# Kernel tuning notes

Measured on AMD Instinct MI355X. Metric: run time of the kernel, lower is better.

## Reference

```python
import jax, jax.numpy as jnp
import numpy as np

NEG_INF = -1e6  # d2l masked_softmax fill value


def setup_inputs() -> dict:
    key = jax.random.key(0)
    ks = jax.random.split(key, 7)
    B, Q, K, D, H = 16, 64, 512, 256, 256
    querys = jax.random.normal(ks[0], (B, Q, D), dtype=jnp.float32)
    keys = jax.random.normal(ks[1], (B, K, D), dtype=jnp.float32)
    values = jax.random.normal(ks[2], (B, K, D), dtype=jnp.float32)
    valid_lens = jax.random.randint(ks[3], (B,), 1, K + 1)
    # learned parameters (Linear weights stored as (in, out) for x @ W)
    Wq = jax.random.normal(ks[4], (D, H), dtype=jnp.float32) / np.sqrt(D)
    Wk = jax.random.normal(ks[5], (D, H), dtype=jnp.float32) / np.sqrt(D)
    w_v = jax.random.normal(ks[6], (H,), dtype=jnp.float32) / np.sqrt(H)
    return {"querys": querys, "keys": keys, "values": values,
            "valid_lens": valid_lens, "Wq": Wq, "Wk": Wk, "w_v": w_v}


def reference(querys, keys, values, valid_lens, Wq, Wk, w_v):
    B, Q, _ = querys.shape
    K = keys.shape[1]
    q = querys @ Wq                      # (B, Q, H)
    k = keys @ Wk                        # (B, K, H)
    features = jnp.tanh(q[:, :, None, :] + k[:, None, :, :])   # (B, Q, K, H)
    scores = jnp.einsum('bqkh,h->bqk', features, w_v)           # (B, Q, K)
    # masked softmax over key axis: positions >= valid_len get -1e6
    mask = jnp.arange(K)[None, None, :] < valid_lens[:, None, None]  # (B,1,K)
    scores = jnp.where(mask, scores, NEG_INF)
    attn = jax.nn.softmax(scores, axis=-1)                       # (B, Q, K)
    return jnp.einsum('bqk,bkd->bqd', attn, values)              # (B, Q, D)
```

## Files before the change

kernel.cpp:

```cpp
#include <hip/hip_runtime.h>

#define BB 16
#define QQ 64
#define KK 512
#define DD 256
#define HH 256
#define KTILE 128
#define NZ 4
#define PERSIST 2048
#define LDST 56

#define LOG2E2 2.88539008177792681f

typedef unsigned int uint;
typedef unsigned short ushort;
typedef __attribute__((ext_vector_type(8))) short bf16x8;
typedef __attribute__((ext_vector_type(8))) unsigned short ushort8;
typedef __attribute__((ext_vector_type(4))) float f32x4;

__device__ __forceinline__ float fast_exp2(float x) {
#if __has_builtin(__builtin_amdgcn_exp2f)
    return __builtin_amdgcn_exp2f(x);
#else
    return exp2f(x);
#endif
}

__device__ __forceinline__ ushort f32_to_bf16_rtne(float x) {
    uint u = __float_as_uint(x);
    u = (u + 0x7FFFu + ((u >> 16) & 1u)) >> 16;
    return (ushort)u;
}

__device__ __forceinline__ void cvt8(uint4 u, float4& a, float4& b) {
    a.x = __uint_as_float(u.x << 16); a.y = __uint_as_float(u.x & 0xFFFF0000u);
    a.z = __uint_as_float(u.y << 16); a.w = __uint_as_float(u.y & 0xFFFF0000u);
    b.x = __uint_as_float(u.z << 16); b.y = __uint_as_float(u.z & 0xFFFF0000u);
    b.z = __uint_as_float(u.w << 16); b.w = __uint_as_float(u.w & 0xFFFF0000u);
}

__global__ __launch_bounds__(256) void proj_both(
        const float* __restrict__ Xq, const float* __restrict__ Wq, float* __restrict__ Yq,
        const float* __restrict__ Xk, const float* __restrict__ Wk, ushort* __restrict__ Yk16,
        const int* __restrict__ valid_lens) {
    __shared__ ushort As[64 * LDST];
    __shared__ ushort Bt[64 * LDST];
    const int rt = blockIdx.x;
    const bool is_q = (rt < 16);
    const float* X; const float* W; int row0;
    if (is_q) { X = Xq; W = Wq; row0 = rt * 64; }
    else {
        X = Xk; W = Wk; row0 = (rt - 16) * 64;
        const int bb    = row0 >> 9;
        const int local = row0 & 511;
        if (local >= valid_lens[bb]) return;
    }
    const int col0 = blockIdx.y * 64;
    const int tid  = threadIdx.x;
    const int lane = tid & 63;
    const int w    = tid >> 6;

    f32x4 acc[4] = {{0.f,0.f,0.f,0.f}, {0.f,0.f,0.f,0.f},
                    {0.f,0.f,0.f,0.f}, {0.f,0.f,0.f,0.f}};

    const int ar = tid >> 2;
    const int ak = (tid & 3) * 8;
    const int bc = tid & 15;
    const int bk = tid >> 4;

    for (int k0 = 0; k0 < HH; k0 += 32) {
        {
            const float* xp = X + (size_t)(row0 + ar) * HH + k0 + ak;
            float4 x0 = *(const float4*)(xp);
            float4 x1 = *(const float4*)(xp + 4);
            ushort8 o;
            o[0] = f32_to_bf16_rtne(x0.x); o[1] = f32_to_bf16_rtne(x0.y);
            o[2] = f32_to_bf16_rtne(x0.z); o[3] = f32_to_bf16_rtne(x0.w);
            o[4] = f32_to_bf16_rtne(x1.x); o[5] = f32_to_bf16_rtne(x1.y);
            o[6] = f32_to_bf16_rtne(x1.z); o[7] = f32_to_bf16_rtne(x1.w);
            *(ushort8*)(&As[ar * LDST + ak]) = o;
        }
        {
            #pragma unroll
            for (int s = 0; s < 2; ++s) {
                float4 wv = *(const float4*)(W + (size_t)(k0 + bk + 16*s) * HH + col0 + bc*4);
                Bt[(bc*4 + 0) * LDST + bk + 16*s] = f32_to_bf16_rtne(wv.x);
                Bt[(bc*4 + 1) * LDST + bk + 16*s] = f32_to_bf16_rtne(wv.y);
                Bt[(bc*4 + 2) * LDST + bk + 16*s] = f32_to_bf16_rtne(wv.z);
                Bt[(bc*4 + 3) * LDST + bk + 16*s] = f32_to_bf16_rtne(wv.w);
            }
        }
        __syncthreads();

        const bf16x8 af = *(const bf16x8*)(&As[(w*16 + (lane & 15)) * LDST + (lane >> 4) * 8]);
        #pragma unroll
        for (int ct = 0; ct < 4; ++ct) {
            const bf16x8 bf = *(const bf16x8*)(&Bt[(ct*16 + (lane & 15)) * LDST + (lane >> 4) * 8]);
            acc[ct] = __builtin_amdgcn_mfma_f32_16x16x32_bf16(af, bf, acc[ct], 0, 0, 0);
        }
        __syncthreads();
    }

    const int orow = row0 + w*16 + (lane >> 4) * 4;
    const int ocol = col0 + (lane & 15);
    if (is_q) {
        #pragma unroll
        for (int ct = 0; ct < 4; ++ct)
            #pragma unroll
            for (int j = 0; j < 4; ++j)
                Yq[(size_t)(orow + j) * HH + ocol + ct*16] = acc[ct][j] * LOG2E2;
    } else {
        #pragma unroll
        for (int ct = 0; ct < 4; ++ct)
            #pragma unroll
            for (int j = 0; j < 4; ++j)
                Yk16[(size_t)(orow + j) * HH + ocol + ct*16] =
                    f32_to_bf16_rtne(acc[ct][j] * LOG2E2);
    }
}

__global__ __launch_bounds__(256) void fused_flash(
        const float* __restrict__ qf, const ushort* __restrict__ kf16,
        const float* __restrict__ w_v, const int* __restrict__ valid_lens,
        const float* __restrict__ values,
        float* __restrict__ pm, float* __restrict__ pl, float* __restrict__ po) {
    __shared__ float sc[2][KTILE];
    __shared__ float pp[2][KTILE];
    __shared__ float red[4][2][DD];

    const int tid  = threadIdx.x;
    const int lane = tid & 63;
    const int w    = tid >> 6;
    const int hg   = lane & 15;
    const int ksub = lane >> 4;
    const int h0   = hg * 16;

    float4 nw[4];
    float wvsum = 0.f;
    #pragma unroll
    for (int i = 0; i < 4; ++i) {
        float4 wv4 = *(const float4*)(w_v + h0 + i*4);
        wvsum += ((wv4.x + wv4.y) + (wv4.z + wv4.w));
        nw[i] = make_float4(-2.f*wv4.x, -2.f*wv4.y, -2.f*wv4.z, -2.f*wv4.w);
    }

    int TT = 0;
    #pragma unroll
    for (int i = 0; i < BB; ++i)
        TT += (valid_lens[i] + KTILE - 1) >> 7;
    const int items = TT * 32;
    const int qch   = items >> 11;
    const int rch   = items & 2047;
    const int bid   = blockIdx.x;
    const int lo_it = bid * qch + ((bid < rch) ? bid : rch);
    const int n_it  = qch + ((bid < rch) ? 1 : 0);

    for (int t = lo_it; t < lo_it + n_it; ++t) {
        const int tile_idx = t >> 5;
        const int q0       = (t & 31) * 2;

        int bb = 0, zz = 0, vlb = 1, acc = 0;
        #pragma unroll
        for (int i = 0; i < BB; ++i) {
            const int v   = valid_lens[i];
            const int nzi = (v + KTILE - 1) >> 7;
            const bool hit = (tile_idx >= acc) && (tile_idx < acc + nzi);
            if (hit) { bb = i; zz = tile_idx - acc; vlb = v; }
            acc += nzi;
        }

        const int tile_lo = zz * KTILE;
        const int tile_hi = (tile_lo + KTILE < vlb) ? (tile_lo + KTILE) : vlb;

        sc[tid >> 7][tid & 127] = -1e6f;

        float4 qA[4], qB[4];
        {
            const float* qrA = qf + (size_t)(bb*QQ + q0) * HH + h0;
            const float* qrB = qrA + HH;
            #pragma unroll
            for (int i = 0; i < 4; ++i) {
                qA[i] = *(const float4*)(qrA + i*4);
                qB[i] = *(const float4*)(qrB + i*4);
            }
        }

        const int lo  = tile_lo + w * 32;
        int hi = lo + 32; hi = (hi > tile_hi) ? tile_hi : hi;
        const int cnt = hi - lo;
        const int ng  = (cnt <= 0) ? 0 : ((cnt + 3) >> 2);

        __syncthreads();

        {
            const size_t brows = (size_t)bb * KK;
            uint4 c0, c1;
            if (ng > 0) {
                int row = lo + ksub;
                row = (row < tile_hi) ? row : (tile_hi - 1);
                const ushort* p = kf16 + (brows + row) * HH + h0;
                c0 = *(const uint4*)(p);
                c1 = *(const uint4*)(p + 8);
            }
            for (int g = 0; g < ng; ++g) {
                uint4 n0, n1;
                const bool more = (g + 1 < ng);
                if (more) {
                    int row = lo + (g+1)*4 + ksub;
                    row = (row < tile_hi) ? row : (tile_hi - 1);
                    const ushort* p = kf16 + (brows + row) * HH + h0;
                    n0 = *(const uint4*)(p);
                    n1 = *(const uint4*)(p + 8);
                }
                float4 kv[4];
                cvt8(c0, kv[0], kv[1]);
                cvt8(c1, kv[2], kv[3]);

                float a0 = wvsum, a1 = 0.f, a2 = 0.f, a3 = 0.f;
                float b0 = wvsum, b1 = 0.f, b2 = 0.f, b3 = 0.f;
                #pragma unroll
                for (int i = 0; i < 4; ++i) {
                    float eA0 = fast_exp2(qA[i].x + kv[i].x);
                    float eA1 = fast_exp2(qA[i].y + kv[i].y);
                    float eA2 = fast_exp2(qA[i].z + kv[i].z);
                    float eA3 = fast_exp2(qA[i].w + kv[i].w);
                    a0 = fmaf(nw[i].x, __builtin_amdgcn_rcpf(eA0 + 1.f), a0);
                    a1 = fmaf(nw[i].y, __builtin_amdgcn_rcpf(eA1 + 1.f), a1);
                    a2 = fmaf(nw[i].z, __builtin_amdgcn_rcpf(eA2 + 1.f), a2);
                    a3 = fmaf(nw[i].w, __builtin_amdgcn_rcpf(eA3 + 1.f), a3);
                    float eB0 = fast_exp2(qB[i].x + kv[i].x);
                    float eB1 = fast_exp2(qB[i].y + kv[i].y);
                    float eB2 = fast_exp2(qB[i].z + kv[i].z);
                    float eB3 = fast_exp2(qB[i].w + kv[i].w);
                    b0 = fmaf(nw[i].x, __builtin_amdgcn_rcpf(eB0 + 1.f), b0);
                    b1 = fmaf(nw[i].y, __builtin_amdgcn_rcpf(eB1 + 1.f), b1);
                    b2 = fmaf(nw[i].z, __builtin_amdgcn_rcpf(eB2 + 1.f), b2);
                    b3 = fmaf(nw[i].w, __builtin_amdgcn_rcpf(eB3 + 1.f), b3);
                }
                float sA = (a0 + a1) + (a2 + a3);
                float sB = (b0 + b1) + (b2 + b3);
                #pragma unroll
                for (int off = 8; off; off >>= 1) {
                    sA += __shfl_xor(sA, off);
                    sB += __shfl_xor(sB, off);
                }
                const int k = lo + g*4 + ksub;
                if (hg == 0 && k < hi) {
                    sc[0][k - tile_lo] = sA;
                    sc[1][k - tile_lo] = sB;
                }
                if (more) { c0 = n0; c1 = n1; }
            }
        }
        __syncthreads();

        if (w < 2) {
            float s0 = sc[w][lane*2], s1 = sc[w][lane*2 + 1];
            float m = fmaxf(s0, s1);
            #pragma unroll
            for (int off = 32; off; off >>= 1) m = fmaxf(m, __shfl_xor(m, off));
            float p0 = __expf(s0 - m), p1 = __expf(s1 - m);
            float l = p0 + p1;
            #pragma unroll
            for (int off = 32; off; off >>= 1) l += __shfl_xor(l, off);
            pp[w][lane*2]     = p0;
            pp[w][lane*2 + 1] = p1;
            if (lane == 0) {
                const int id = ((bb*QQ + q0 + w) << 2) + zz;
                pm[id] = m; pl[id] = l;
            }
        }
        __syncthreads();

        {
            const float* V = values + (size_t)bb * KK * DD + lane*4;
            float4 aA = make_float4(0.f,0.f,0.f,0.f);
            float4 aB = aA;
            #pragma unroll 4
            for (int k = lo; k < hi; ++k) {
                const float pA = pp[0][k - tile_lo];
                const float pB = pp[1][k - tile_lo];
                float4 v4 = *(const float4*)(V + (size_t)k * DD);
                aA.x = fmaf(pA, v4.x, aA.x); aA.y = fmaf(pA, v4.y, aA.y);
                aA.z = fmaf(pA, v4.z, aA.z); aA.w = fmaf(pA, v4.w, aA.w);
                aB.x = fmaf(pB, v4.x, aB.x); aB.y = fmaf(pB, v4.y, aB.y);
                aB.z = fmaf(pB, v4.z, aB.z); aB.w = fmaf(pB, v4.w, aB.w);
            }
            *(float4*)(&red[w][0][lane*4]) = aA;
            *(float4*)(&red[w][1][lane*4]) = aB;
        }
        __syncthreads();

        #pragma unroll
        for (int i = 0; i < 2; ++i) {
            const int idx = tid + i*256;
            const int qq = idx >> 8, d = idx & 255;
            const float o = (red[0][qq][d] + red[1][qq][d])
                          + (red[2][qq][d] + red[3][qq][d]);
            po[(size_t)(((bb*QQ + q0 + qq) << 2) + zz) * DD + d] = o;
        }
        __syncthreads();
    }
}

__global__ __launch_bounds__(256) void combine_kernel(
        const float* __restrict__ pm, const float* __restrict__ pl,
        const float* __restrict__ po, const int* __restrict__ valid_lens,
        float* __restrict__ out) {
    const int b   = blockIdx.x;
    const int q   = blockIdx.y;
    const int tid = threadIdx.x;
    const int vl  = valid_lens[b];
    const int nz  = (vl + KTILE - 1) >> 7;
    const int idx4 = (b*QQ + q) << 2;

    float mz[NZ], wz[NZ];
    float M = -3.0e38f;
    #pragma unroll
    for (int z = 0; z < NZ; ++z) {
        mz[z] = (z < nz) ? pm[idx4 + z] : -3.0e38f;
        M = fmaxf(M, mz[z]);
    }
    float L = 0.f;
    #pragma unroll
    for (int z = 0; z < NZ; ++z) {
        wz[z] = (z < nz) ? __expf(mz[z] - M) : 0.f;
        L = fmaf(wz[z], (z < nz) ? pl[idx4 + z] : 0.f, L);
    }
    const float inv = 1.f / L;

    float o = 0.f;
    #pragma unroll
    for (int z = 0; z < NZ; ++z) {
        if (z < nz)
            o = fmaf(wz[z], po[(size_t)(idx4 + z) * DD + tid], o);
    }
    out[(size_t)(b*QQ + q) * DD + tid] = o * inv;
}

extern "C" void kernel_launch(void* const* d_in, const int* in_sizes, int n_in,
                              void* d_out, int out_size, void* d_ws, size_t ws_size,
                              hipStream_t stream) {
    (void)in_sizes; (void)n_in; (void)out_size; (void)ws_size;
    const float* querys     = (const float*)d_in[0];
    const float* keys       = (const float*)d_in[1];
    const float* values     = (const float*)d_in[2];
    const int*   valid_lens = (const int*)d_in[3];
    const float* Wq         = (const float*)d_in[4];
    const float* Wk         = (const float*)d_in[5];
    const float* w_v        = (const float*)d_in[6];
    float* out = (float*)d_out;

    float*  qf    = (float*)d_ws;
    ushort* kfeat = (ushort*)(qf + (size_t)BB*QQ*HH);
    float*  pm    = (float*)(kfeat + (size_t)BB*KK*HH);
    float*  pl    = pm + BB*QQ*NZ;
    float*  po    = pl + BB*QQ*NZ;

    proj_both<<<dim3(16 + BB*KK/64, HH/64), 256, 0, stream>>>(
        querys, Wq, qf, keys, Wk, kfeat, valid_lens);
    fused_flash<<<dim3(PERSIST), 256, 0, stream>>>(
        qf, kfeat, w_v, valid_lens, values, pm, pl, po);
    combine_kernel<<<dim3(BB, QQ), 256, 0, stream>>>(
        pm, pl, po, valid_lens, out);
}
```

Baseline: 44.24 us.

## Process eight queries per block with XCD-aware tile mapping instead of persistent loop

Replaces the persistent grid-stride loop over (tile, query-pair) items with one work item per block: each block handles a 128-key tile for 8 queries, and block IDs are mapped so that tiles are grouped by XCD (blockIdx & 7). Query features are staged in shared memory, and each loaded key row and value row is reused across 8 queries instead of 2. This cuts key/value reloads and L2 traffic. In exchange, shared memory use and register pressure go up, and blocks with tl >= TT exit early, leaving some of the grid idle.

```diff
diff --git a/kernel.cpp b/kernel.cpp
--- a/kernel.cpp
+++ b/kernel.cpp
@@ -7,7 +7,6 @@
 #define HH 256
 #define KTILE 128
 #define NZ 4
-#define PERSIST 2048
 #define LDST 56
 
 #define LOG2E2 2.88539008177792681f
@@ -124,9 +123,10 @@
         const float* __restrict__ w_v, const int* __restrict__ valid_lens,
         const float* __restrict__ values,
         float* __restrict__ pm, float* __restrict__ pl, float* __restrict__ po) {
-    __shared__ float sc[2][KTILE];
-    __shared__ float pp[2][KTILE];
-    __shared__ float red[4][2][DD];
+    __shared__ float qls[8][16][20];
+    __shared__ float sc[8][KTILE];
+    __shared__ float pp[8][KTILE];
+    __shared__ float red[4][8][DD];
 
     const int tid  = threadIdx.x;
     const int lane = tid & 63;
@@ -135,6 +135,30 @@
     const int ksub = lane >> 4;
     const int h0   = hg * 16;
 
+    int TT = 0;
+    #pragma unroll
+    for (int i = 0; i < BB; ++i)
+        TT += (valid_lens[i] + KTILE - 1) >> 7;
+
+    const int xcd = blockIdx.x & 7;
+    const int j   = blockIdx.x >> 3;
+    const int tl  = xcd + 8 * (j >> 3);
+    const int oct = j & 7;
+    if (tl >= TT) return;
+    const int q0 = oct * 8;
+
+    int bb = 0, zz = 0, vlb = 1, acc = 0;
+    #pragma unroll
+    for (int i = 0; i < BB; ++i) {
+        const int v   = valid_lens[i];
+        const int nzi = (v + KTILE - 1) >> 7;
+        const bool hit = (tl >= acc) && (tl < acc + nzi);
+        if (hit) { bb = i; zz = tl - acc; vlb = v; }
+        acc += nzi;
+    }
+    const int tile_lo = zz * KTILE;
+    const int tile_hi = (tile_lo + KTILE < vlb) ? (tile_lo + KTILE) : vlb;
+
     float4 nw[4];
     float wvsum = 0.f;
     #pragma unroll
@@ -144,162 +168,154 @@
         nw[i] = make_float4(-2.f*wv4.x, -2.f*wv4.y, -2.f*wv4.z, -2.f*wv4.w);
     }
 
-    int TT = 0;
-    #pragma unroll
-    for (int i = 0; i < BB; ++i)
-        TT += (valid_lens[i] + KTILE - 1) >> 7;
-    const int items = TT * 32;
-    const int qch   = items >> 11;
-    const int rch   = items & 2047;
-    const int bid   = blockIdx.x;
-    const int lo_it = bid * qch + ((bid < rch) ? bid : rch);
-    const int n_it  = qch + ((bid < rch) ? 1 : 0);
-
-    for (int t = lo_it; t < lo_it + n_it; ++t) {
-        const int tile_idx = t >> 5;
-        const int q0       = (t & 31) * 2;
-
-        int bb = 0, zz = 0, vlb = 1, acc = 0;
-        #pragma unroll
-        for (int i = 0; i < BB; ++i) {
-            const int v   = valid_lens[i];
-            const int nzi = (v + KTILE - 1) >> 7;
-            const bool hit = (tile_idx >= acc) && (tile_idx < acc + nzi);
-            if (hit) { bb = i; zz = tile_idx - acc; vlb = v; }
-            acc += nzi;
-        }
-
-        const int tile_lo = zz * KTILE;
-        const int tile_hi = (tile_lo + KTILE < vlb) ? (tile_lo + KTILE) : vlb;
-
-        sc[tid >> 7][tid & 127] = -1e6f;
-
-        float4 qA[4], qB[4];
-        {
-            const float* qrA = qf + (size_t)(bb*QQ + q0) * HH + h0;
-            const float* qrB = qrA + HH;
-            #pragma unroll
-            for (int i = 0; i < 4; ++i) {
-                qA[i] = *(const float4*)(qrA + i*4);
-                qB[i] = *(const float4*)(qrB + i*4);
-            }
-        }
-
-        const int lo  = tile_lo + w * 32;
-        int hi = lo + 32; hi = (hi > tile_hi) ? tile_hi : hi;
-        const int cnt = hi - lo;
-        const int ng  = (cnt <= 0) ? 0 : ((cnt + 3) >> 2);
-
-        __syncthreads();
-
-        {
-            const size_t brows = (size_t)bb * KK;
-            uint4 c0, c1;
-            if (ng > 0) {
-                int row = lo + ksub;
+    {
+        const int q = tid >> 5, s = tid & 31;
+        const int sh = s >> 1, half = s & 1;
+        const float* qp = qf + (size_t)(bb*QQ + q0 + q) * HH + sh*16 + half*8;
+        float4 xa = *(const float4*)(qp);
+        float4 xb = *(const float4*)(qp + 4);
+        *(float4*)(&qls[q][sh][half*8])     = xa;
+        *(float4*)(&qls[q][sh][half*8 + 4]) = xb;
+    }
+    #pragma unroll
+    for (int i = 0; i < 4; ++i) {
+        const int slot = tid + i*256;
+        sc[slot >> 7][slot & 127] = -1e6f;
+    }
+
+    const int lo  = tile_lo + w * 32;
+    int hi = lo + 32; hi = (hi > tile_hi) ? tile_hi : hi;
+    const int cnt = hi - lo;
+    const int ng  = (cnt <= 0) ? 0 : ((cnt + 3) >> 2);
+
+    __syncthreads();
+
+    {
+        const size_t brows = (size_t)bb * KK;
+        uint4 c0, c1;
+        if (ng > 0) {
+            int row = lo + ksub;
+            row = (row < tile_hi) ? row : (tile_hi - 1);
+            const ushort* p = kf16 + (brows + row) * HH + h0;
+            c0 = *(const uint4*)(p);
+            c1 = *(const uint4*)(p + 8);
+        }
+        for (int g = 0; g < ng; ++g) {
+            uint4 n0, n1;
+            const bool more = (g + 1 < ng);
+            if (more) {
+                int row = lo + (g+1)*4 + ksub;
                 row = (row < tile_hi) ? row : (tile_hi - 1);
                 const ushort* p = kf16 + (brows + row) * HH + h0;
-                c0 = *(const uint4*)(p);
-                c1 = *(const uint4*)(p + 8);
+                n0 = *(const uint4*)(p);
+                n1 = *(const uint4*)(p + 8);
             }
-            for (int g = 0; g < ng; ++g) {
-                uint4 n0, n1;
-                const bool more = (g + 1 < ng);
-                if (more) {
-                    int row = lo + (g+1)*4 + ksub;
-                    row = (row < tile_hi) ? row : (tile_hi - 1);
-                    const ushort* p = kf16 + (brows + row) * HH + h0;
-                    n0 = *(const uint4*)(p);
-                    n1 = *(const uint4*)(p + 8);
+            float4 kv[4];
+            cvt8(c0, kv[0], kv[1]);
+            cvt8(c1, kv[2], kv[3]);
+
+            const int k = lo + g*4 + ksub;
+            #pragma unroll
+            for (int pass = 0; pass < 2; ++pass) {
+                float s4[4];
+                #pragma unroll
+                for (int qi = 0; qi < 4; ++qi) {
+                    const int q = pass*4 + qi;
+                    float a0 = wvsum, a1 = 0.f, a2 = 0.f, a3 = 0.f;
+                    #pragma unroll
+                    for (int i = 0; i < 4; ++i) {
+                        const float4 qv = *(const float4*)(&qls[q][hg][i*4]);
+                        float e0 = fast_exp2(qv.x + kv[i].x);
+                        float e1 = fast_exp2(qv.y + kv[i].y);
+                        float e2 = fast_exp2(qv.z + kv[i].z);
+                        float e3 = fast_exp2(qv.w + kv[i].w);
+                        a0 = fmaf(nw[i].x, __builtin_amdgcn_rcpf(e0 + 1.f), a0);
+                        a1 = fmaf(nw[i].y, __builtin_amdgcn_rcpf(e1 + 1.f), a1);
+                        a2 = fmaf(nw[i].z, __builtin_amdgcn_rcpf(e2 + 1.f), a2);
+                        a3 = fmaf(nw[i].w, __builtin_amdgcn_rcpf(e3 + 1.f), a3);
+                    }
+                    s4[qi] = (a0 + a1) + (a2 + a3);
                 }
-                float4 kv[4];
-                cvt8(c0, kv[0], kv[1]);
-                cvt8(c1, kv[2], kv[3]);
-
-                float a0 = wvsum, a1 = 0.f, a2 = 0.f, a3 = 0.f;
-                float b0 = wvsum, b1 = 0.f, b2 = 0.f, b3 = 0.f;
-                #pragma unroll
-                for (int i = 0; i < 4; ++i) {
-                    float eA0 = fast_exp2(qA[i].x + kv[i].x);
-                    float eA1 = fast_exp2(qA[i].y + kv[i].y);
-                    float eA2 = fast_exp2(qA[i].z + kv[i].z);
-                    float eA3 = fast_exp2(qA[i].w + kv[i].w);
-                    a0 = fmaf(nw[i].x, __builtin_amdgcn_rcpf(eA0 + 1.f), a0);
-                    a1 = fmaf(nw[i].y, __builtin_amdgcn_rcpf(eA1 + 1.f), a1);
-                    a2 = fmaf(nw[i].z, __builtin_amdgcn_rcpf(eA2 + 1.f), a2);
-                    a3 = fmaf(nw[i].w, __builtin_amdgcn_rcpf(eA3 + 1.f), a3);
-                    float eB0 = fast_exp2(qB[i].x + kv[i].x);
-                    float eB1 = fast_exp2(qB[i].y + kv[i].y);
-                    float eB2 = fast_exp2(qB[i].z + kv[i].z);
-                    float eB3 = fast_exp2(qB[i].w + kv[i].w);
-                    b0 = fmaf(nw[i].x, __builtin_amdgcn_rcpf(eB0 + 1.f), b0);
-                    b1 = fmaf(nw[i].y, __builtin_amdgcn_rcpf(eB1 + 1.f), b1);
-                    b2 = fmaf(nw[i].z, __builtin_amdgcn_rcpf(eB2 + 1.f), b2);
-                    b3 = fmaf(nw[i].w, __builtin_amdgcn_rcpf(eB3 + 1.f), b3);
-                }
-                float sA = (a0 + a1) + (a2 + a3);
-                float sB = (b0 + b1) + (b2 + b3);
                 #pragma unroll
                 for (int off = 8; off; off >>= 1) {
-                    sA += __shfl_xor(sA, off);
-                    sB += __shfl_xor(sB, off);
+                    #pragma unroll
+                    for (int qi = 0; qi < 4; ++qi)
+                        s4[qi] += __shfl_xor(s4[qi], off);
                 }
-                const int k = lo + g*4 + ksub;
                 if (hg == 0 && k < hi) {
-                    sc[0][k - tile_lo] = sA;
-                    sc[1][k - tile_lo] = sB;
+                    #pragma unroll
+                    for (int qi = 0; qi < 4; ++qi)
+                        sc[pass*4 + qi][k - tile_lo] = s4[qi];
                 }
-                if (more) { c0 = n0; c1 = n1; }
             }
-        }
-        __syncthreads();
-
-        if (w < 2) {
-            float s0 = sc[w][lane*2], s1 = sc[w][lane*2 + 1];
-            float m = fmaxf(s0, s1);
-            #pragma unroll
-            for (int off = 32; off; off >>= 1) m = fmaxf(m, __shfl_xor(m, off));
-            float p0 = __expf(s0 - m), p1 = __expf(s1 - m);
-            float l = p0 + p1;
-            #pragma unroll
-            for (int off = 32; off; off >>= 1) l += __shfl_xor(l, off);
-            pp[w][lane*2]     = p0;
-            pp[w][lane*2 + 1] = p1;
-            if (lane == 0) {
-                const int id = ((bb*QQ + q0 + w) << 2) + zz;
-                pm[id] = m; pl[id] = l;
-            }
-        }
-        __syncthreads();
-
-        {
-            const float* V = values + (size_t)bb * KK * DD + lane*4;
-            float4 aA = make_float4(0.f,0.f,0.f,0.f);
-            float4 aB = aA;
-            #pragma unroll 4
-            for (int k = lo; k < hi; ++k) {
-                const float pA = pp[0][k - tile_lo];
-                const float pB = pp[1][k - tile_lo];
-                float4 v4 = *(const float4*)(V + (size_t)k * DD);
-                aA.x = fmaf(pA, v4.x, aA.x); aA.y = fmaf(pA, v4.y, aA.y);
-                aA.z = fmaf(pA, v4.z, aA.z); aA.w = fmaf(pA, v4.w, aA.w);
-                aB.x = fmaf(pB, v4.x, aB.x); aB.y = fmaf(pB, v4.y, aB.y);
-                aB.z = fmaf(pB, v4.z, aB.z); aB.w = fmaf(pB, v4.w, aB.w);
-            }
-            *(float4*)(&red[w][0][lane*4]) = aA;
-            *(float4*)(&red[w][1][lane*4]) = aB;
-        }
-        __syncthreads();
-
-        #pragma unroll
-        for (int i = 0; i < 2; ++i) {
-            const int idx = tid + i*256;
-            const int qq = idx >> 8, d = idx & 255;
-            const float o = (red[0][qq][d] + red[1][qq][d])
-                          + (red[2][qq][d] + red[3][qq][d]);
-            po[(size_t)(((bb*QQ + q0 + qq) << 2) + zz) * DD + d] = o;
-        }
-        __syncthreads();
+            if (more) { c0 = n0; c1 = n1; }
+        }
+    }
+    __syncthreads();
+
+    #pragma unroll
+    for (int r = 0; r < 2; ++r) {
+        const int q = 2*w + r;
+        float s0 = sc[q][lane*2], s1 = sc[q][lane*2 + 1];
+        float m = fmaxf(s0, s1);
+        #pragma unroll
+        for (int off = 32; off; off >>= 1) m = fmaxf(m, __shfl_xor(m, off));
+        float p0 = __expf(s0 - m), p1 = __expf(s1 - m);
+        float l = p0 + p1;
+        #pragma unroll
+        for (int off = 32; off; off >>= 1) l += __shfl_xor(l, off);
+        pp[q][lane*2]     = p0;
+        pp[q][lane*2 + 1] = p1;
+        if (lane == 0) {
+            const int id = ((bb*QQ + q0 + q) << 2) + zz;
+            pm[id] = m; pl[id] = l;
+        }
+    }
+    __syncthreads();
+
+    {
+        const float* V = values + (size_t)bb * KK * DD + lane*4;
+        float4 a0 = make_float4(0.f,0.f,0.f,0.f);
+        float4 a1 = a0, a2 = a0, a3 = a0, a4 = a0, a5 = a0, a6 = a0, a7 = a0;
+        for (int k = lo; k < hi; ++k) {
+            const int kt = k - tile_lo;
+            float4 v4 = *(const float4*)(V + (size_t)k * DD);
+            const float w0 = pp[0][kt], w1 = pp[1][kt], w2 = pp[2][kt], w3 = pp[3][kt];
+            const float w4 = pp[4][kt], w5 = pp[5][kt], w6 = pp[6][kt], w7 = pp[7][kt];
+            a0.x = fmaf(w0, v4.x, a0.x); a0.y = fmaf(w0, v4.y, a0.y);
+            a0.z = fmaf(w0, v4.z, a0.z); a0.w = fmaf(w0, v4.w, a0.w);
+            a1.x = fmaf(w1, v4.x, a1.x); a1.y = fmaf(w1, v4.y, a1.y);
+            a1.z = fmaf(w1, v4.z, a1.z); a1.w = fmaf(w1, v4.w, a1.w);
+            a2.x = fmaf(w2, v4.x, a2.x); a2.y = fmaf(w2, v4.y, a2.y);
+            a2.z = fmaf(w2, v4.z, a2.z); a2.w = fmaf(w2, v4.w, a2.w);
+            a3.x = fmaf(w3, v4.x, a3.x); a3.y = fmaf(w3, v4.y, a3.y);
+            a3.z = fmaf(w3, v4.z, a3.z); a3.w = fmaf(w3, v4.w, a3.w);
+            a4.x = fmaf(w4, v4.x, a4.x); a4.y = fmaf(w4, v4.y, a4.y);
+            a4.z = fmaf(w4, v4.z, a4.z); a4.w = fmaf(w4, v4.w, a4.w);
+            a5.x = fmaf(w5, v4.x, a5.x); a5.y = fmaf(w5, v4.y, a5.y);
+            a5.z = fmaf(w5, v4.z, a5.z); a5.w = fmaf(w5, v4.w, a5.w);
+            a6.x = fmaf(w6, v4.x, a6.x); a6.y = fmaf(w6, v4.y, a6.y);
+            a6.z = fmaf(w6, v4.z, a6.z); a6.w = fmaf(w6, v4.w, a6.w);
+            a7.x = fmaf(w7, v4.x, a7.x); a7.y = fmaf(w7, v4.y, a7.y);
+            a7.z = fmaf(w7, v4.z, a7.z); a7.w = fmaf(w7, v4.w, a7.w);
+        }
+        *(float4*)(&red[w][0][lane*4]) = a0;
+        *(float4*)(&red[w][1][lane*4]) = a1;
+        *(float4*)(&red[w][2][lane*4]) = a2;
+        *(float4*)(&red[w][3][lane*4]) = a3;
+        *(float4*)(&red[w][4][lane*4]) = a4;
+        *(float4*)(&red[w][5][lane*4]) = a5;
+        *(float4*)(&red[w][6][lane*4]) = a6;
+        *(float4*)(&red[w][7][lane*4]) = a7;
+    }
+    __syncthreads();
+
+    #pragma unroll
+    for (int i = 0; i < 8; ++i) {
+        const int slot = tid + i*256;
+        const int q = slot >> 8, d = slot & 255;
+        const float o = (red[0][q][d] + red[1][q][d]) + (red[2][q][d] + red[3][q][d]);
+        po[(size_t)(((bb*QQ + q0 + q) << 2) + zz) * DD + d] = o;
     }
 }
 
@@ -359,7 +375,7 @@
 
     proj_both<<<dim3(16 + BB*KK/64, HH/64), 256, 0, stream>>>(
         querys, Wq, qf, keys, Wk, kfeat, valid_lens);
-    fused_flash<<<dim3(PERSIST), 256, 0, stream>>>(
+    fused_flash<<<dim3(2048), 256, 0, stream>>>(
         qf, kfeat, w_v, valid_lens, values, pm, pl, po);
     combine_kernel<<<dim3(BB, QQ), 256, 0, stream>>>(
         pm, pl, po, valid_lens, out);
```

Measured after the change: 50.96 us. +15.2%, slower.
